# Performance work log

Hardware: AMD Instinct MI355X
Metric: run time of the kernel (lower is better)

Reference implementation:

```python
import jax, jax.numpy as jnp
import numpy as np
import math

L, V, D, H, TBLK = 12, 50257, 768, 12, 1024
HD = D // H
EPS = 1e-5


def setup_inputs() -> dict:
    key = jax.random.key(0)
    ks = jax.random.split(key, 16)
    B, T = 2, 1024
    s = 0.02
    idx = jax.random.randint(ks[0], (B, T), 0, V, dtype=jnp.int32)
    inp = {
        "idx": idx,
        "wte": jax.random.normal(ks[1], (V, D), jnp.float32) * s,
        "wpe": jax.random.normal(ks[2], (TBLK, D), jnp.float32) * s,
        # per-layer params stacked along leading L axis
        "ln1_g": jnp.ones((L, D), jnp.float32),
        "ln1_b": jnp.zeros((L, D), jnp.float32),
        "attn_w": jax.random.normal(ks[3], (L, D, 3 * D), jnp.float32) * s,
        "attn_b": jnp.zeros((L, 3 * D), jnp.float32),
        "aproj_w": jax.random.normal(ks[4], (L, D, D), jnp.float32) * s,
        "aproj_b": jnp.zeros((L, D), jnp.float32),
        "ln2_g": jnp.ones((L, D), jnp.float32),
        "ln2_b": jnp.zeros((L, D), jnp.float32),
        "fc_w": jax.random.normal(ks[5], (L, D, 4 * D), jnp.float32) * s,
        "fc_b": jnp.zeros((L, 4 * D), jnp.float32),
        "mproj_w": jax.random.normal(ks[6], (L, 4 * D, D), jnp.float32) * s,
        "mproj_b": jnp.zeros((L, D), jnp.float32),
        "lnf_g": jnp.ones((D,), jnp.float32),
        "lnf_b": jnp.zeros((D,), jnp.float32),
        "lm_w": jax.random.normal(ks[7], (D, V), jnp.float32) * s,  # lm_head weight (stored transposed)
    }
    return inp


def _layer_norm(x, g, b):
    mu = jnp.mean(x, axis=-1, keepdims=True)
    var = jnp.mean(jnp.square(x - mu), axis=-1, keepdims=True)
    return (x - mu) * jax.lax.rsqrt(var + EPS) * g + b


def _block(x, p):
    (ln1g, ln1b, aw, ab, pw, pb, ln2g, ln2b, fw, fb, mw, mb) = p
    B, T, C = x.shape
    h = _layer_norm(x, ln1g, ln1b)
    qkv = h @ aw + ab  # [B,T,3D]
    q, k, v = jnp.split(qkv, 3, axis=-1)
    q = q.reshape(B, T, H, HD)
    k = k.reshape(B, T, H, HD)
    v = v.reshape(B, T, H, HD)
    scores = jnp.einsum('bihd,bjhd->bhij', q, k) * (1.0 / math.sqrt(HD))
    mask = jnp.tril(jnp.ones((T, T), bool))
    scores = jnp.where(mask, scores, jnp.float32(-jnp.inf))
    attn = jax.nn.softmax(scores, axis=-1)
    o = jnp.einsum('bhij,bjhd->bihd', attn, v).reshape(B, T, C)
    x = x + o @ pw + pb
    h = _layer_norm(x, ln2g, ln2b)
    h = jax.nn.gelu(h @ fw + fb, approximate=True)
    x = x + h @ mw + mb
    return x, None


def reference(idx, wte, wpe, ln1_g, ln1_b, attn_w, attn_b, aproj_w, aproj_b,
              ln2_g, ln2_b, fc_w, fc_b, mproj_w, mproj_b, lnf_g, lnf_b, lm_w):
    B, T = idx.shape
    x = wte[idx] + wpe[jnp.arange(T)]
    layers = (ln1_g, ln1_b, attn_w, attn_b, aproj_w, aproj_b,
              ln2_g, ln2_b, fc_w, fc_b, mproj_w, mproj_b)
    x, _ = jax.lax.scan(_block, x, layers)
    x = _layer_norm(x, lnf_g, lnf_b)
    logits = x @ lm_w  # [B,T,V]
    return logits
```

## Files before the change

### kernel.cpp

```cpp
#include <hip/hip_runtime.h>
#include <hip/hip_bf16.h>
#include <math.h>

#define BT_   2048
#define D_    768
#define T_    1024
#define H_    12
#define HD_   64
#define L_    12
#define V_    50257
#define VPAD_ 50304
#define NCHUNK_ 7168

typedef __hip_bfloat16 bf16;
typedef short bf16x8 __attribute__((ext_vector_type(8)));
typedef float f32x4 __attribute__((ext_vector_type(4)));

__global__ __launch_bounds__(256) void embed_kernel(const int* __restrict__ idx,
                                                    const float* __restrict__ wte,
                                                    const float* __restrict__ wpe,
                                                    float* __restrict__ x) {
    int bt = blockIdx.x;
    int t  = bt & (T_ - 1);
    int tok = idx[bt];
    const float* wrow = wte + (size_t)tok * D_;
    const float* prow = wpe + (size_t)t * D_;
    float* xrow = x + (size_t)bt * D_;
    for (int d = threadIdx.x; d < D_; d += 256)
        xrow[d] = wrow[d] + prow[d];
}

__global__ __launch_bounds__(256) void lnorm_kernel(const float* __restrict__ in,
                                                    const float* __restrict__ g,
                                                    const float* __restrict__ b,
                                                    bf16* __restrict__ out) {
    int row = blockIdx.x;
    const float* xr = in + (size_t)row * D_;
    float s = 0.f, s2 = 0.f;
    for (int d = threadIdx.x; d < D_; d += 256) {
        float v = xr[d];
        s += v; s2 += v * v;
    }
    #pragma unroll
    for (int o = 32; o >= 1; o >>= 1) {
        s  += __shfl_xor(s,  o);
        s2 += __shfl_xor(s2, o);
    }
    __shared__ float ss[4], ss2[4];
    int wid = threadIdx.x >> 6;
    if ((threadIdx.x & 63) == 0) { ss[wid] = s; ss2[wid] = s2; }
    __syncthreads();
    s  = ss[0] + ss[1] + ss[2] + ss[3];
    s2 = ss2[0] + ss2[1] + ss2[2] + ss2[3];
    float mu  = s / D_;
    float var = s2 / D_ - mu * mu;
    float rstd = rsqrtf(var + 1e-5f);
    bf16* orow = out + (size_t)row * D_;
    for (int d = threadIdx.x; d < D_; d += 256)
        orow[d] = __float2bfloat16((xr[d] - mu) * rstd * g[d] + b[d]);
}

__global__ __launch_bounds__(256) void convT_kernel(const float* __restrict__ W,
                                                    bf16* __restrict__ Wt,
                                                    int K, int ldW, int n_src0, int Nreal,
                                                    size_t sW, size_t sT) {
    W  += (size_t)blockIdx.z * sW;
    Wt += (size_t)blockIdx.z * sT;
    __shared__ float t[32][33];
    int tx = threadIdx.x & 31, ty = threadIdx.x >> 5;
    int k0 = blockIdx.y * 32, n0 = blockIdx.x * 32;
    #pragma unroll
    for (int i = 0; i < 4; i++) {
        int k = k0 + ty + i * 8;
        int n = n_src0 + n0 + tx;
        t[ty + i * 8][tx] = (n < Nreal) ? W[(size_t)k * ldW + n] : 0.f;
    }
    __syncthreads();
    #pragma unroll
    for (int i = 0; i < 4; i++)
        Wt[(size_t)(n0 + ty + i * 8) * K + k0 + tx] = __float2bfloat16(t[tx][ty + i * 8]);
}

__device__ inline float gelu_f(float v) {
    const float c = 0.7978845608028654f;
    float u = c * (v + 0.044715f * v * v * v);
    return 0.5f * v * (1.f + tanhf(u));
}

__device__ inline void gload16(const void* g, void* l) {
    __builtin_amdgcn_global_load_lds((const __attribute__((address_space(1))) void*)g,
                                     (__attribute__((address_space(3))) void*)l, 16, 0, 0);
}

template <int BM, int BN, int WM, int WN, int EPI, int NGRP, typename OT>
__device__ __attribute__((always_inline)) void gemm_body(
        const bf16* __restrict__ A, const bf16* __restrict__ Bt,
        const float* __restrict__ bias, const float* res, OT* C,
        int K, int ldC, int n_off, int Ncap, int nx) {
    constexpr int NW = WM * WN;
    constexpr int MI = BM / WM / 16;
    constexpr int NJ = BN / WN / 16;
    constexpr int GA = (BM / 16) / NW;
    constexpr int GB = (BN / 16) / NW;
    constexpr int G  = GA + GB;
    static_assert(GA >= 1 && GB >= 1, "stage mapping needs >=1 seg per wave");
    __shared__ __align__(16) short smem[3 * (BM + BN) * 32];
    short* Asm = smem;
    short* Bsm = smem + 3 * BM * 32;
    const int tid  = threadIdx.x;
    const int lane = tid & 63;
    const int wid  = tid >> 6;
    const int wm = wid / WN, wn = wid % WN;

    const int nwg = gridDim.x;
    const int bid = blockIdx.x;
    const int q8  = nwg >> 3, r8 = nwg & 7;
    const int xcd = bid & 7, off = bid >> 3;
    const int swz = (xcd < r8 ? xcd * (q8 + 1) : r8 * (q8 + 1) + (xcd - r8) * q8) + off;
    int m0, n0;
    if constexpr (NGRP > 0) {
        const int Gsz = nx * NGRP;
        const int g = swz / Gsz, r = swz % Gsz;
        m0 = (r % nx) * BM;
        n0 = (g * NGRP + r / nx) * BN;
    } else {
        m0 = (swz % nx) * BM;
        n0 = (swz / nx) * BN;
    }

    const int rS = lane >> 2;
    const int cS = ((lane & 3) ^ ((lane >> 3) & 3)) * 8;
    const int fr = lane & 15;
    const int fq = lane >> 4;
    const int rc = (fq ^ ((fr >> 1) & 3)) * 8;

    auto STAGE = [&](int buf, int k0) {
        #pragma unroll
        for (int s = 0; s < GA; s++) {
            const int seg = wid * GA + s;
            gload16(A + (size_t)(m0 + seg * 16 + rS) * K + k0 + cS, &Asm[buf * BM * 32 + seg * 512]);
        }
        #pragma unroll
        for (int s = 0; s < GB; s++) {
            const int seg = wid * GB + s;
            gload16(Bt + (size_t)(n0 + seg * 16 + rS) * K + k0 + cS, &Bsm[buf * BN * 32 + seg * 512]);
        }
    };

    f32x4 acc[MI][NJ] = {};

    auto COMPUTE = [&](int buf) {
        bf16x8 af[MI], bfr[NJ];
        #pragma unroll
        for (int i = 0; i < MI; i++)
            af[i] = *(const bf16x8*)&Asm[buf * BM * 32 + (wm * (BM / WM) + i * 16 + fr) * 32 + rc];
        #pragma unroll
        for (int j = 0; j < NJ; j++)
            bfr[j] = *(const bf16x8*)&Bsm[buf * BN * 32 + (wn * (BN / WN) + j * 16 + fr) * 32 + rc];
        #pragma unroll
        for (int i = 0; i < MI; i++)
            #pragma unroll
            for (int j = 0; j < NJ; j++)
                acc[i][j] = __builtin_amdgcn_mfma_f32_16x16x32_bf16(af[i], bfr[j], acc[i][j], 0, 0, 0);
    };

    const int nk = K / 32;
    STAGE(0, 0);
    STAGE(1, 32);
    int cur = 0;
    for (int ks = 0; ks < nk - 1; ks++) {
        asm volatile("s_waitcnt vmcnt(%0)" :: "n"(G) : "memory");
        __builtin_amdgcn_s_barrier();
        __builtin_amdgcn_sched_barrier(0);
        if (ks + 2 < nk) {
            int nxt = cur + 2; if (nxt >= 3) nxt -= 3;
            STAGE(nxt, (ks + 2) * 32);
        }
        COMPUTE(cur);
        cur = (cur + 1 == 3) ? 0 : cur + 1;
    }
    asm volatile("s_waitcnt vmcnt(0)" ::: "memory");
    __builtin_amdgcn_s_barrier();
    __builtin_amdgcn_sched_barrier(0);
    COMPUTE(cur);

    #pragma unroll
    for (int j = 0; j < NJ; j++) {
        const int col = n_off + n0 + wn * (BN / WN) + j * 16 + fr;
        if (col >= Ncap) continue;
        const float bb = (EPI == 3) ? 0.f : bias[col];
        #pragma unroll
        for (int i = 0; i < MI; i++) {
            #pragma unroll
            for (int r = 0; r < 4; r++) {
                const int row = m0 + wm * (BM / WM) + i * 16 + fq * 4 + r;
                float v = acc[i][j][r] + bb;
                if (EPI == 1) v += res[(size_t)row * ldC + col];
                if (EPI == 2) v = gelu_f(v);
                if constexpr (sizeof(OT) == 2)
                    C[(size_t)row * ldC + col] = __float2bfloat16(v);
                else
                    C[(size_t)row * ldC + col] = v;
            }
        }
    }
}

__global__ __launch_bounds__(256) void gemm_qkv(const bf16* A, const bf16* Bt, const float* bias,
                                                const float* res, bf16* C, int K, int ldC,
                                                int n_off, int Ncap, int nx) {
    gemm_body<128, 64, 2, 2, 0, 0, bf16>(A, Bt, bias, res, C, K, ldC, n_off, Ncap, nx);
}
__global__ __launch_bounds__(256) void gemm_aproj(const bf16* A, const bf16* Bt, const float* bias,
                                                  const float* res, float* C, int K, int ldC,
                                                  int n_off, int Ncap, int nx) {
    gemm_body<64, 64, 2, 2, 1, 0, float>(A, Bt, bias, res, C, K, ldC, n_off, Ncap, nx);
}
__global__ __launch_bounds__(256) void gemm_fc(const bf16* A, const bf16* Bt, const float* bias,
                                               const float* res, bf16* C, int K, int ldC,
                                               int n_off, int Ncap, int nx) {
    gemm_body<128, 64, 2, 2, 2, 0, bf16>(A, Bt, bias, res, C, K, ldC, n_off, Ncap, nx);
}
__global__ __launch_bounds__(256) void gemm_mproj(const bf16* A, const bf16* Bt, const float* bias,
                                                  const float* res, float* C, int K, int ldC,
                                                  int n_off, int Ncap, int nx) {
    gemm_body<64, 64, 2, 2, 1, 0, float>(A, Bt, bias, res, C, K, ldC, n_off, Ncap, nx);
}
__global__ __launch_bounds__(512) void gemm_lmhead(const bf16* A, const bf16* Bt, const float* bias,
                                                   const float* res, float* C, int K, int ldC,
                                                   int n_off, int Ncap, int nx) {
    gemm_body<128, 128, 4, 2, 3, 4, float>(A, Bt, bias, res, C, K, ldC, n_off, Ncap, nx);
}

__device__ inline unsigned pk_bf16(float a, float b) {
    __hip_bfloat16 ha = __float2bfloat16(a), hb = __float2bfloat16(b);
    unsigned short ua = *(unsigned short*)&ha, ub = *(unsigned short*)&hb;
    return (unsigned)ua | ((unsigned)ub << 16);
}

__global__ __launch_bounds__(256) void fattn_kernel(const bf16* __restrict__ qkv,
                                                    bf16* __restrict__ att) {
    const int qi  = 15 - blockIdx.x;
    const int bh  = blockIdx.y;
    const int h   = bh % H_;
    const int b   = bh / H_;
    const int q0  = qi * 64;
    const int tid = threadIdx.x;
    const int lane = tid & 63;
    const int w   = tid >> 6;
    const int fr  = lane & 15;
    const int fq  = lane >> 4;

    __shared__ __align__(16) short K_lds[64 * 64];
    __shared__ __align__(16) short Vt_lds[64 * 64];
    __shared__ __align__(16) short P_lds[4][16 * 80];

    const size_t base = (size_t)b * T_ * 2304;
    const int qrow = q0 + w * 16 + fr;

    bf16x8 qf[2];
    qf[0] = *(const bf16x8*)(qkv + base + (size_t)qrow * 2304 + h * 64 + fq * 8);
    qf[1] = *(const bf16x8*)(qkv + base + (size_t)qrow * 2304 + h * 64 + 32 + fq * 8);

    const int vj  = tid >> 2;
    const int vd0 = (tid & 3) * 16;

    f32x4 acc[4] = {};
    float m = -1e30f, l = 0.f;

    const int nt = qi + 1;
    for (int kt = 0; kt < nt; kt++) {
        const int j0 = kt * 64;

        #pragma unroll
        for (int p = 0; p < 2; p++) {
            const int jl  = p * 32 + w * 8 + (lane >> 3);
            const int chg = (lane & 7) ^ (jl & 7);
            gload16(qkv + base + (size_t)(j0 + jl) * 2304 + D_ + h * 64 + chg * 8,
                    &K_lds[(p * 32 + w * 8) * 64]);
        }
        {
            const bf16* vsrc = qkv + base + (size_t)(j0 + vj) * 2304 + 2 * D_ + h * 64 + vd0;
            bf16x8 v0 = *(const bf16x8*)vsrc;
            bf16x8 v1 = *(const bf16x8*)(vsrc + 8);
            #pragma unroll
            for (int e = 0; e < 8; e++) {
                Vt_lds[((vd0 + e) * 64 + vj) ^ (e << 3)]     = v0[e];
                Vt_lds[((vd0 + 8 + e) * 64 + vj) ^ (e << 3)] = v1[e];
            }
        }
        __syncthreads();

        f32x4 s[4];
        #pragma unroll
        for (int jb = 0; jb < 4; jb++) {
            const int j = jb * 16 + fr;
            bf16x8 k0 = *(const bf16x8*)&K_lds[j * 64 + (((0 + fq) ^ (fr & 7)) << 3)];
            bf16x8 k1 = *(const bf16x8*)&K_lds[j * 64 + (((4 + fq) ^ (fr & 7)) << 3)];
            f32x4 z = {};
            z = __builtin_amdgcn_mfma_f32_16x16x32_bf16(k0, qf[0], z, 0, 0, 0);
            s[jb] = __builtin_amdgcn_mfma_f32_16x16x32_bf16(k1, qf[1], z, 0, 0, 0);
        }

        const bool need_mask = (j0 + 63 > q0 + w * 16);
        float mx = -1e30f;
        #pragma unroll
        for (int jb = 0; jb < 4; jb++) {
            #pragma unroll
            for (int r = 0; r < 4; r++) {
                float v = s[jb][r] * 0.125f;
                if (need_mask && (j0 + jb * 16 + fq * 4 + r > qrow)) v = -1e30f;
                s[jb][r] = v;
                mx = fmaxf(mx, v);
            }
        }
        mx = fmaxf(mx, __shfl_xor(mx, 16));
        mx = fmaxf(mx, __shfl_xor(mx, 32));

        const float mnew  = fmaxf(m, mx);
        const float alpha = __expf(m - mnew);

        float ts = 0.f;
        #pragma unroll
        for (int jb = 0; jb < 4; jb++) {
            #pragma unroll
            for (int r = 0; r < 4; r++) {
                s[jb][r] = __expf(s[jb][r] - mnew);
                ts += s[jb][r];
            }
            *(unsigned*)&P_lds[w][fr * 80 + jb * 16 + fq * 4]     = pk_bf16(s[jb][0], s[jb][1]);
            *(unsigned*)&P_lds[w][fr * 80 + jb * 16 + fq * 4 + 2] = pk_bf16(s[jb][2], s[jb][3]);
        }
        ts += __shfl_xor(ts, 16);
        ts += __shfl_xor(ts, 32);
        l = l * alpha + ts;
        #pragma unroll
        for (int db = 0; db < 4; db++)
            #pragma unroll
            for (int r = 0; r < 4; r++) acc[db][r] *= alpha;
        m = mnew;

        bf16x8 pa0 = *(const bf16x8*)&P_lds[w][fr * 80 + fq * 8];
        bf16x8 pa1 = *(const bf16x8*)&P_lds[w][fr * 80 + 32 + fq * 8];
        #pragma unroll
        for (int db = 0; db < 4; db++) {
            const int d = db * 16 + fr;
            bf16x8 vt0 = *(const bf16x8*)&Vt_lds[(d * 64 + fq * 8) ^ ((fr & 7) << 3)];
            bf16x8 vt1 = *(const bf16x8*)&Vt_lds[(d * 64 + 32 + fq * 8) ^ ((fr & 7) << 3)];
            acc[db] = __builtin_amdgcn_mfma_f32_16x16x32_bf16(vt0, pa0, acc[db], 0, 0, 0);
            acc[db] = __builtin_amdgcn_mfma_f32_16x16x32_bf16(vt1, pa1, acc[db], 0, 0, 0);
        }
        __syncthreads();
    }

    const float inv_l = 1.f / l;
    bf16* orow = att + (size_t)(b * T_ + qrow) * D_ + h * 64;
    #pragma unroll
    for (int db = 0; db < 4; db++) {
        #pragma unroll
        for (int rp = 0; rp < 2; rp++) {
            unsigned u = pk_bf16(acc[db][rp * 2] * inv_l, acc[db][rp * 2 + 1] * inv_l);
            *(unsigned*)(orow + db * 16 + fq * 4 + rp * 2) = u;
        }
    }
}

extern "C" void kernel_launch(void* const* d_in, const int* in_sizes, int n_in,
                              void* d_out, int out_size, void* d_ws, size_t ws_size,
                              hipStream_t stream) {
    const int* idx      = (const int*)  d_in[0];
    const float* wte    = (const float*)d_in[1];
    const float* wpe    = (const float*)d_in[2];
    const float* ln1_g  = (const float*)d_in[3];
    const float* ln1_b  = (const float*)d_in[4];
    const float* attn_w = (const float*)d_in[5];
    const float* attn_b = (const float*)d_in[6];
    const float* aproj_w= (const float*)d_in[7];
    const float* aproj_b= (const float*)d_in[8];
    const float* ln2_g  = (const float*)d_in[9];
    const float* ln2_b  = (const float*)d_in[10];
    const float* fc_w   = (const float*)d_in[11];
    const float* fc_b   = (const float*)d_in[12];
    const float* mproj_w= (const float*)d_in[13];
    const float* mproj_b= (const float*)d_in[14];
    const float* lnf_g  = (const float*)d_in[15];
    const float* lnf_b  = (const float*)d_in[16];
    const float* lm_w   = (const float*)d_in[17];
    float* out = (float*)d_out;

    char* wsB = (char*)d_ws;
    float* x   = (float*)(wsB);
    bf16*  big = (bf16*) (wsB + 6291456);
    bf16*  hbuf= (bf16*) (wsB + 18874368);
    bf16*  att = (bf16*) (wsB + 22020096);

    const size_t S_QKV = (size_t)2304 * 768, S_AP = (size_t)768 * 768;
    const size_t S_FC  = (size_t)3072 * 768, S_MP = (size_t)3072 * 768;
    const bool big_ws = ws_size >= 272302080ull;

    embed_kernel<<<BT_, 256, 0, stream>>>(idx, wte, wpe, x);

    if (big_ws) {
        bf16* w_qkv  = (bf16*)(wsB + 25165824);
        bf16* w_ap   = w_qkv + S_QKV * L_;
        bf16* w_fc   = w_ap  + S_AP  * L_;
        bf16* w_mp   = w_fc  + S_FC  * L_;
        bf16* lm_wt  = w_mp  + S_MP  * L_;

        convT_kernel<<<dim3(72, 24, L_), 256, 0, stream>>>(attn_w, w_qkv, 768, 2304, 0, 2304, S_QKV, S_QKV);
        convT_kernel<<<dim3(24, 24, L_), 256, 0, stream>>>(aproj_w, w_ap, 768, 768, 0, 768, S_AP, S_AP);
        convT_kernel<<<dim3(96, 24, L_), 256, 0, stream>>>(fc_w, w_fc, 768, 3072, 0, 3072, S_FC, S_FC);
        convT_kernel<<<dim3(24, 96, L_), 256, 0, stream>>>(mproj_w, w_mp, 3072, 768, 0, 768, S_MP, S_MP);
        convT_kernel<<<dim3(VPAD_ / 32, 24, 1), 256, 0, stream>>>(lm_w, lm_wt, 768, V_, 0, V_, 0, 0);

        for (int l = 0; l < L_; l++) {
            lnorm_kernel<<<BT_, 256, 0, stream>>>(x, ln1_g + (size_t)l * D_, ln1_b + (size_t)l * D_, hbuf);
            gemm_qkv<<<16 * 36, 256, 0, stream>>>(
                hbuf, w_qkv + l * S_QKV, attn_b + (size_t)l * 3 * D_, nullptr, big, 768, 2304, 0, 2304, 16);
            fattn_kernel<<<dim3(16, 2 * H_), 256, 0, stream>>>(big, att);
            gemm_aproj<<<32 * 12, 256, 0, stream>>>(
                att, w_ap + l * S_AP, aproj_b + (size_t)l * D_, x, x, 768, 768, 0, 768, 32);
            lnorm_kernel<<<BT_, 256, 0, stream>>>(x, ln2_g + (size_t)l * D_, ln2_b + (size_t)l * D_, hbuf);
            gemm_fc<<<16 * 48, 256, 0, stream>>>(
                hbuf, w_fc + l * S_FC, fc_b + (size_t)l * 4 * D_, nullptr, big, 768, 3072, 0, 3072, 16);
            gemm_mproj<<<32 * 12, 256, 0, stream>>>(
                big, w_mp + l * S_MP, mproj_b + (size_t)l * D_, x, x, 3072, 768, 0, 768, 32);
        }

        lnorm_kernel<<<BT_, 256, 0, stream>>>(x, lnf_g, lnf_b, hbuf);
        gemm_lmhead<<<16 * (VPAD_ / 128), 512, 0, stream>>>(
            hbuf, lm_wt, nullptr, nullptr, out, 768, V_, 0, V_, 16);
    } else {
        bf16* wbuf    = (bf16*)(wsB + 25165824);
        bf16* w_qkv   = wbuf;
        bf16* w_ap    = wbuf + S_QKV;
        bf16* w_fc    = w_ap + S_AP;
        bf16* w_mp    = w_fc + S_FC;

        for (int l = 0; l < L_; l++) {
            lnorm_kernel<<<BT_, 256, 0, stream>>>(x, ln1_g + (size_t)l * D_, ln1_b + (size_t)l * D_, hbuf);
            convT_kernel<<<dim3(72, 24, 1), 256, 0, stream>>>(
                attn_w + l * S_QKV, w_qkv, 768, 2304, 0, 2304, 0, 0);
            gemm_qkv<<<16 * 36, 256, 0, stream>>>(
                hbuf, w_qkv, attn_b + (size_t)l * 3 * D_, nullptr, big, 768, 2304, 0, 2304, 16);
            fattn_kernel<<<dim3(16, 2 * H_), 256, 0, stream>>>(big, att);
            convT_kernel<<<dim3(24, 24, 1), 256, 0, stream>>>(
                aproj_w + l * S_AP, w_ap, 768, 768, 0, 768, 0, 0);
            gemm_aproj<<<32 * 12, 256, 0, stream>>>(
                att, w_ap, aproj_b + (size_t)l * D_, x, x, 768, 768, 0, 768, 32);
            lnorm_kernel<<<BT_, 256, 0, stream>>>(x, ln2_g + (size_t)l * D_, ln2_b + (size_t)l * D_, hbuf);
            convT_kernel<<<dim3(96, 24, 1), 256, 0, stream>>>(
                fc_w + l * S_FC, w_fc, 768, 3072, 0, 3072, 0, 0);
            gemm_fc<<<16 * 48, 256, 0, stream>>>(
                hbuf, w_fc, fc_b + (size_t)l * 4 * D_, nullptr, big, 768, 3072, 0, 3072, 16);
            convT_kernel<<<dim3(24, 96, 1), 256, 0, stream>>>(
                mproj_w + l * S_MP, w_mp, 3072, 768, 0, 768, 0, 0);
            gemm_mproj<<<32 * 12, 256, 0, stream>>>(
                big, w_mp, mproj_b + (size_t)l * D_, x, x, 3072, 768, 0, 768, 32);
        }

        lnorm_kernel<<<BT_, 256, 0, stream>>>(x, lnf_g, lnf_b, hbuf);
        for (int c0 = 0; c0 < VPAD_; c0 += NCHUNK_) {
            int ncnt = (VPAD_ - c0 < NCHUNK_) ? (VPAD_ - c0) : NCHUNK_;
            convT_kernel<<<dim3(ncnt / 32, 24, 1), 256, 0, stream>>>(
                lm_w, wbuf, 768, V_, c0, V_, 0, 0);
            gemm_lmhead<<<16 * (ncnt / 128), 512, 0, stream>>>(
                hbuf, wbuf, nullptr, nullptr, out, 768, V_, c0, V_, 16);
        }
    }
}
```

Before: 2.181 ms.

## Use 64-deep K tiles in per-layer GEMMs with XOR-swizzled LDS staging

Adds a new GEMM body that stages 64-wide K slices per pipeline step (triple-buffered via global_load_lds) instead of 32. Each stage issues two MFMA 16x16x32 per output tile, halving the number of barriers and waitcnt syncs per K loop. Switches the qkv, attention-projection, fc and mlp-projection kernels to it; the lm_head kernel keeps the old path. The cost is doubled LDS per block, which may reduce occupancy, and more registers for fragments.

Result: faster. 2.046 ms (-6.2%).

```diff
diff --git a/kernel.cpp b/kernel.cpp
--- a/kernel.cpp
+++ b/kernel.cpp
@@ -90,6 +90,126 @@
 __device__ inline void gload16(const void* g, void* l) {
     __builtin_amdgcn_global_load_lds((const __attribute__((address_space(1))) void*)g,
                                      (__attribute__((address_space(3))) void*)l, 16, 0, 0);
+}
+
+template <int BM, int BN, int WM, int WN, int EPI, typename OT>
+__device__ __attribute__((always_inline)) void gemm_body64(
+        const bf16* __restrict__ A, const bf16* __restrict__ Bt,
+        const float* __restrict__ bias, const float* res, OT* C,
+        int K, int ldC, int n_off, int Ncap, int nx) {
+    constexpr int NW = WM * WN;
+    constexpr int MI = BM / WM / 16;
+    constexpr int NJ = BN / WN / 16;
+    constexpr int SA = (BM / 16) / NW;
+    constexpr int SB = (BN / 16) / NW;
+    constexpr int G  = 2 * (SA + SB);
+    static_assert(SA >= 1 && SB >= 1, "stage mapping needs >=1 seg per wave");
+    __shared__ __align__(16) short smem[3 * (BM + BN) * 64];
+    short* Asm = smem;
+    short* Bsm = smem + 3 * BM * 64;
+    const int tid  = threadIdx.x;
+    const int lane = tid & 63;
+    const int wid  = tid >> 6;
+    const int wm = wid / WN, wn = wid % WN;
+
+    const int nwg = gridDim.x;
+    const int bid = blockIdx.x;
+    const int q8  = nwg >> 3, r8 = nwg & 7;
+    const int xcd = bid & 7, off = bid >> 3;
+    const int swz = (xcd < r8 ? xcd * (q8 + 1) : r8 * (q8 + 1) + (xcd - r8) * q8) + off;
+    const int m0 = (swz % nx) * BM;
+    const int n0 = (swz / nx) * BN;
+
+    const int rS8 = lane >> 3;
+    const int cS  = ((lane & 7) ^ rS8) * 8;
+    const int fr = lane & 15;
+    const int fq = lane >> 4;
+
+    auto STAGE = [&](int buf, int k0) {
+        #pragma unroll
+        for (int s = 0; s < SA; s++) {
+            const int seg = wid * SA + s;
+            #pragma unroll
+            for (int g = 0; g < 2; g++)
+                gload16(A + (size_t)(m0 + seg * 16 + g * 8 + rS8) * K + k0 + cS,
+                        &Asm[buf * BM * 64 + seg * 1024 + g * 512]);
+        }
+        #pragma unroll
+        for (int s = 0; s < SB; s++) {
+            const int seg = wid * SB + s;
+            #pragma unroll
+            for (int g = 0; g < 2; g++)
+                gload16(Bt + (size_t)(n0 + seg * 16 + g * 8 + rS8) * K + k0 + cS,
+                        &Bsm[buf * BN * 64 + seg * 1024 + g * 512]);
+        }
+    };
+
+    f32x4 acc[MI][NJ] = {};
+
+    auto COMPUTE = [&](int buf) {
+        bf16x8 af[2][MI], bfr[2][NJ];
+        #pragma unroll
+        for (int kh = 0; kh < 2; kh++) {
+            #pragma unroll
+            for (int i = 0; i < MI; i++) {
+                const int row = wm * (BM / WM) + i * 16 + fr;
+                af[kh][i] = *(const bf16x8*)&Asm[buf * BM * 64 + row * 64 + (((kh * 4 + fq) ^ (fr & 7)) << 3)];
+            }
+            #pragma unroll
+            for (int j = 0; j < NJ; j++) {
+                const int row = wn * (BN / WN) + j * 16 + fr;
+                bfr[kh][j] = *(const bf16x8*)&Bsm[buf * BN * 64 + row * 64 + (((kh * 4 + fq) ^ (fr & 7)) << 3)];
+            }
+        }
+        #pragma unroll
+        for (int i = 0; i < MI; i++)
+            #pragma unroll
+            for (int j = 0; j < NJ; j++) {
+                acc[i][j] = __builtin_amdgcn_mfma_f32_16x16x32_bf16(af[0][i], bfr[0][j], acc[i][j], 0, 0, 0);
+                acc[i][j] = __builtin_amdgcn_mfma_f32_16x16x32_bf16(af[1][i], bfr[1][j], acc[i][j], 0, 0, 0);
+            }
+    };
+
+    const int nk = K / 64;
+    STAGE(0, 0);
+    STAGE(1, 64);
+    int cur = 0;
+    for (int ks = 0; ks < nk - 1; ks++) {
+        asm volatile("s_waitcnt vmcnt(%0)" :: "n"(G) : "memory");
+        __builtin_amdgcn_s_barrier();
+        __builtin_amdgcn_sched_barrier(0);
+        if (ks + 2 < nk) {
+            int nxt = cur + 2; if (nxt >= 3) nxt -= 3;
+            STAGE(nxt, (ks + 2) * 64);
+        }
+        COMPUTE(cur);
+        cur = (cur + 1 == 3) ? 0 : cur + 1;
+    }
+    asm volatile("s_waitcnt vmcnt(0)" ::: "memory");
+    __builtin_amdgcn_s_barrier();
+    __builtin_amdgcn_sched_barrier(0);
+    COMPUTE(cur);
+
+    #pragma unroll
+    for (int j = 0; j < NJ; j++) {
+        const int col = n_off + n0 + wn * (BN / WN) + j * 16 + fr;
+        if (col >= Ncap) continue;
+        const float bb = (EPI == 3) ? 0.f : bias[col];
+        #pragma unroll
+        for (int i = 0; i < MI; i++) {
+            #pragma unroll
+            for (int r = 0; r < 4; r++) {
+                const int row = m0 + wm * (BM / WM) + i * 16 + fq * 4 + r;
+                float v = acc[i][j][r] + bb;
+                if (EPI == 1) v += res[(size_t)row * ldC + col];
+                if (EPI == 2) v = gelu_f(v);
+                if constexpr (sizeof(OT) == 2)
+                    C[(size_t)row * ldC + col] = __float2bfloat16(v);
+                else
+                    C[(size_t)row * ldC + col] = v;
+            }
+        }
+    }
 }
 
 template <int BM, int BN, int WM, int WN, int EPI, int NGRP, typename OT>
@@ -209,22 +329,22 @@
 __global__ __launch_bounds__(256) void gemm_qkv(const bf16* A, const bf16* Bt, const float* bias,
                                                 const float* res, bf16* C, int K, int ldC,
                                                 int n_off, int Ncap, int nx) {
-    gemm_body<128, 64, 2, 2, 0, 0, bf16>(A, Bt, bias, res, C, K, ldC, n_off, Ncap, nx);
+    gemm_body64<128, 64, 2, 2, 0, bf16>(A, Bt, bias, res, C, K, ldC, n_off, Ncap, nx);
 }
 __global__ __launch_bounds__(256) void gemm_aproj(const bf16* A, const bf16* Bt, const float* bias,
                                                   const float* res, float* C, int K, int ldC,
                                                   int n_off, int Ncap, int nx) {
-    gemm_body<64, 64, 2, 2, 1, 0, float>(A, Bt, bias, res, C, K, ldC, n_off, Ncap, nx);
+    gemm_body64<64, 64, 2, 2, 1, float>(A, Bt, bias, res, C, K, ldC, n_off, Ncap, nx);
 }
 __global__ __launch_bounds__(256) void gemm_fc(const bf16* A, const bf16* Bt, const float* bias,
                                                const float* res, bf16* C, int K, int ldC,
                                                int n_off, int Ncap, int nx) {
-    gemm_body<128, 64, 2, 2, 2, 0, bf16>(A, Bt, bias, res, C, K, ldC, n_off, Ncap, nx);
+    gemm_body64<128, 64, 2, 2, 2, bf16>(A, Bt, bias, res, C, K, ldC, n_off, Ncap, nx);
 }
 __global__ __launch_bounds__(256) void gemm_mproj(const bf16* A, const bf16* Bt, const float* bias,
                                                   const float* res, float* C, int K, int ldC,
                                                   int n_off, int Ncap, int nx) {
-    gemm_body<64, 64, 2, 2, 1, 0, float>(A, Bt, bias, res, C, K, ldC, n_off, Ncap, nx);
+    gemm_body64<64, 64, 2, 2, 1, float>(A, Bt, bias, res, C, K, ldC, n_off, Ncap, nx);
 }
 __global__ __launch_bounds__(512) void gemm_lmhead(const bf16* A, const bf16* Bt, const float* bias,
                                                    const float* res, float* C, int K, int ldC,
```
